# Performance work log

Hardware: AMD Instinct MI355X
Metric: run time of the kernel (lower is better)

The kernel has to match this reference:

```python
import jax, jax.numpy as jnp
from jax import lax
import numpy as np

B, DIM, H, W = 32, 256, 64, 64
HEADS = 4


def _dwconv(x, w, b, pad):
    # depthwise conv: w is (gc, 1, kh, kw), feature_group_count = gc
    y = lax.conv_general_dilated(x, w, window_strides=(1, 1), padding=pad,
                                 feature_group_count=w.shape[0])
    return y + b[None, :, None, None]


def setup_inputs() -> dict:
    key = jax.random.key(0)
    ks = jax.random.split(key, 9)
    gc = (DIM // 2) // 8  # branch_ratio = 0.125 -> 16
    s = 0.1
    return {
        "x": jax.random.normal(ks[0], (B, DIM, H, W), dtype=jnp.float32),
        "w_hw": jax.random.normal(ks[1], (gc, 1, 3, 3), dtype=jnp.float32) * s,
        "b_hw": jax.random.normal(ks[2], (gc,), dtype=jnp.float32) * s,
        "w_w": jax.random.normal(ks[3], (gc, 1, 1, 11), dtype=jnp.float32) * s,
        "b_w": jax.random.normal(ks[4], (gc,), dtype=jnp.float32) * s,
        "w_h": jax.random.normal(ks[5], (gc, 1, 11, 1), dtype=jnp.float32) * s,
        "b_h": jax.random.normal(ks[6], (gc,), dtype=jnp.float32) * s,
        "w_qkvl": jax.random.normal(ks[7], (DIM // 4 * HEADS, DIM // 2), dtype=jnp.float32) * s,
        "b_qkvl": jax.random.normal(ks[8], (DIM // 4 * HEADS,), dtype=jnp.float32) * s,
    }


def reference(x, w_hw, b_hw, w_w, b_w, w_h, b_h, w_qkvl, b_qkvl):
    Bx, C, Hx, Wx = x.shape
    C4 = C // 4
    gc = w_hw.shape[0]
    n_id = C // 2 - 3 * gc
    x1, x2 = jnp.split(x, 2, axis=1)  # each (B, C/2, H, W)

    # --- local branch: Inception depthwise conv + GELU ---
    xid = x1[:, :n_id]
    xhw = x1[:, n_id:n_id + gc]
    xw = x1[:, n_id + gc:n_id + 2 * gc]
    xh = x1[:, n_id + 2 * gc:]
    x1 = jnp.concatenate([
        xid,
        _dwconv(xhw, w_hw, b_hw, ((1, 1), (1, 1))),
        _dwconv(xw, w_w, b_w, ((0, 0), (5, 5))),
        _dwconv(xh, w_h, b_h, ((5, 5), (0, 0))),
    ], axis=1)
    x1 = jax.nn.gelu(x1, approximate=False)

    # --- global branch: 1x1 conv -> GELU -> pooled channel attention ---
    x2 = jnp.einsum('bchw,oc->bohw', x2, w_qkvl) + b_qkvl[None, :, None, None]
    x2 = jax.nn.gelu(x2, approximate=False)
    x2 = x2.reshape(Bx, HEADS, C4, Hx, Wx)

    q = jnp.sum(x2[:, :HEADS - 3], axis=1)          # (B, C4, H, W)
    k = x2[:, HEADS - 3]                             # (B, C4, H, W)
    v = x2[:, HEADS - 2].reshape(Bx, C4, Hx * Wx)    # (B, C4, HW)
    lfeat = x2[:, HEADS - 1]                         # (B, C4, H, W)

    # AvgPool2d(k=3, s=2, p=1) with count_include_pad=True (torch default)
    qp = lax.reduce_window(q, 0.0, lax.add, (1, 1, 3, 3), (1, 1, 2, 2),
                           ((0, 0), (0, 0), (1, 1), (1, 1))) / 9.0
    # MaxPool2d(k=2, s=2, p=0)
    kp = lax.reduce_window(k, -jnp.inf, lax.max, (1, 1, 2, 2), (1, 1, 2, 2), 'VALID')

    qf = qp.reshape(Bx, C4, -1)  # (B, C4, Np)
    kf = kp.reshape(Bx, C4, -1)  # (B, C4, Np)

    qk = jnp.einsum('bcn,bdn->bcd', qf, kf)          # (B, C4, C4)
    attn = jax.nn.softmax(qk, axis=1)                # softmax over dim=1, as in torch
    # torch: softmax(qk,1).transpose(1,2) @ v  ==  einsum over c
    out = jnp.einsum('bcd,bcm->bdm', attn, v).reshape(Bx, C4, Hx, Wx)

    return jnp.concatenate([x1, lfeat, out], axis=1)
```

## Files before the change

### kernel.cpp

```cpp
#include <hip/hip_runtime.h>
#include <hip/hip_bf16.h>

constexpr int kB   = 32;
constexpr int kC   = 256;
constexpr int kHW  = 4096;
constexpr int kC4  = 64;
constexpr int kGC  = 16;
constexpr int kNID = 80;

__device__ __forceinline__ float gelu_exact(float x) {
    return 0.5f * x * (1.0f + erff(x * 0.70710678118654752440f));
}

__device__ __forceinline__ float4 gelu4(float4 v) {
    return make_float4(gelu_exact(v.x), gelu_exact(v.y), gelu_exact(v.z), gelu_exact(v.w));
}

__global__ __launch_bounds__(256) void init_kernel(float4* __restrict__ qp, float4* __restrict__ qkb)
{
    int bid = blockIdx.x;
    if (bid < 2048) {
        size_t i = (size_t)bid * 256 + threadIdx.x;
        qp[i] = make_float4(0.f, 0.f, 0.f, 0.f);
    } else {
        size_t i = (size_t)(bid - 2048) * 256 + threadIdx.x;
        qkb[i] = make_float4(0.f, 0.f, 0.f, 0.f);
    }
}

__global__ __launch_bounds__(256) void part1_kernel(
    const float* __restrict__ x,
    const float* __restrict__ w_hw, const float* __restrict__ b_hw,
    const float* __restrict__ w_w,  const float* __restrict__ b_w,
    const float* __restrict__ w_h,  const float* __restrict__ b_h,
    float* __restrict__ out)
{
    int bc = blockIdx.x;
    int b  = bc >> 7;
    int c  = bc & 127;
    const float4* xp4 = (const float4*)(x   + (size_t)(b * kC + c) * kHW);
    float4*       op4 = (float4*)      (out + (size_t)(b * kC + c) * kHW);
    int tid = threadIdx.x;

    if (c < kNID) {
        for (int q = tid; q < 1024; q += 256)
            op4[q] = gelu4(xp4[q]);
    } else if (c < kNID + kGC) {
        int g = c - kNID;
        float wv[9];
        #pragma unroll
        for (int j = 0; j < 9; ++j) wv[j] = w_hw[g * 9 + j];
        float bias = b_hw[g];
        for (int q = tid; q < 1024; q += 256) {
            int h = q >> 4, wq = q & 15;
            float ax = bias, ay = bias, az = bias, aw = bias;
            #pragma unroll
            for (int dy = -1; dy <= 1; ++dy) {
                int rr = h + dy;
                if ((unsigned)rr >= 64u) continue;
                int base = rr * 16;
                float  l  = (wq > 0)  ? xp4[base + wq - 1].w : 0.f;
                float4 Bv = xp4[base + wq];
                float  r  = (wq < 15) ? xp4[base + wq + 1].x : 0.f;
                float w0 = wv[(dy + 1) * 3 + 0];
                float w1 = wv[(dy + 1) * 3 + 1];
                float w2 = wv[(dy + 1) * 3 + 2];
                ax += w0 * l    + w1 * Bv.x + w2 * Bv.y;
                ay += w0 * Bv.x + w1 * Bv.y + w2 * Bv.z;
                az += w0 * Bv.y + w1 * Bv.z + w2 * Bv.w;
                aw += w0 * Bv.z + w1 * Bv.w + w2 * r;
            }
            op4[q] = make_float4(gelu_exact(ax), gelu_exact(ay), gelu_exact(az), gelu_exact(aw));
        }
    } else if (c < kNID + 2 * kGC) {
        int g = c - (kNID + kGC);
        float wv[11];
        #pragma unroll
        for (int j = 0; j < 11; ++j) wv[j] = w_w[g * 11 + j];
        float bias = b_w[g];
        for (int q = tid; q < 1024; q += 256) {
            int h = q >> 4, wq = q & 15;
            int base = h * 16;
            float f[20];
            #pragma unroll
            for (int m = 0; m < 5; ++m) {
                int qq = wq + m - 2;
                float4 v;
                if ((unsigned)qq < 16u) v = xp4[base + qq];
                else                    v = make_float4(0.f, 0.f, 0.f, 0.f);
                f[4 * m + 0] = v.x; f[4 * m + 1] = v.y;
                f[4 * m + 2] = v.z; f[4 * m + 3] = v.w;
            }
            float a0 = bias, a1 = bias, a2 = bias, a3 = bias;
            #pragma unroll
            for (int m = 0; m < 11; ++m) {
                float w = wv[m];
                a0 += w * f[m + 3];
                a1 += w * f[m + 4];
                a2 += w * f[m + 5];
                a3 += w * f[m + 6];
            }
            op4[q] = make_float4(gelu_exact(a0), gelu_exact(a1), gelu_exact(a2), gelu_exact(a3));
        }
    } else {
        int g = c - (kNID + 2 * kGC);
        float wv[11];
        #pragma unroll
        for (int j = 0; j < 11; ++j) wv[j] = w_h[g * 11 + j];
        float bias = b_h[g];
        for (int q = tid; q < 1024; q += 256) {
            int h = q >> 4, wq = q & 15;
            float a0 = bias, a1 = bias, a2 = bias, a3 = bias;
            #pragma unroll
            for (int m = 0; m < 11; ++m) {
                int rr = h + m - 5;
                if ((unsigned)rr < 64u) {
                    float4 v = xp4[rr * 16 + wq];
                    float w = wv[m];
                    a0 += w * v.x; a1 += w * v.y; a2 += w * v.z; a3 += w * v.w;
                }
            }
            op4[q] = make_float4(gelu_exact(a0), gelu_exact(a1), gelu_exact(a2), gelu_exact(a3));
        }
    }
}

__global__ __launch_bounds__(256, 3) void conv1x1_kernel(
    const float* __restrict__ x,
    const float* __restrict__ w_qkvl, const float* __restrict__ b_qkvl,
    float* __restrict__ qp, float* __restrict__ kp,
    float* __restrict__ out)
{
    __shared__ float Ws[32][64];
    __shared__ float Xs[32 * 256];
    int pb   = blockIdx.x;
    int p0   = pb * 256;
    int head = blockIdx.y;
    int o0   = head * 64;
    int b    = blockIdx.z;
    int t    = threadIdx.x;
    int og   = t >> 5;
    int tp   = t & 31;

    float acc[8][8] = {};
    for (int kc = 0; kc < 4; ++kc) {
        #pragma unroll
        for (int r = 0; r < 2; ++r) {
            int g = t + r * 256;
            int o = g & 63, kq = g >> 6;
            float4 w4 = *(const float4*)&w_qkvl[(size_t)(o0 + o) * 128 + kc * 32 + kq * 4];
            Ws[kq * 4 + 0][o] = w4.x;
            Ws[kq * 4 + 1][o] = w4.y;
            Ws[kq * 4 + 2][o] = w4.z;
            Ws[kq * 4 + 3][o] = w4.w;
        }
        #pragma unroll
        for (int r = 0; r < 8; ++r) {
            int g = t + r * 256;
            int k = g >> 6, cch = g & 63;
            int cph = (cch >> 1) + (cch & 1) * 32;
            *(float4*)&Xs[k * 256 + cph * 4] =
                *(const float4*)&x[(size_t)(b * kC + 128 + kc * 32 + k) * kHW + p0 + cch * 4];
        }
        __syncthreads();
        #pragma unroll 2
        for (int k = 0; k < 32; ++k) {
            const float* xrow = &Xs[k * 256];
            float4 wa = *(const float4*)&Ws[k][og * 8];
            float4 wb = *(const float4*)&Ws[k][og * 8 + 4];
            float4 xa = *(const float4*)&xrow[tp * 4];
            float4 xb = *(const float4*)&xrow[128 + tp * 4];
            float w8[8] = {wa.x, wa.y, wa.z, wa.w, wb.x, wb.y, wb.z, wb.w};
            float x8[8] = {xa.x, xa.y, xa.z, xa.w, xb.x, xb.y, xb.z, xb.w};
            #pragma unroll
            for (int i = 0; i < 8; ++i)
                #pragma unroll
                for (int j = 0; j < 8; ++j)
                    acc[i][j] += w8[i] * x8[j];
        }
        __syncthreads();
    }

    if (head < 2) {
        float* Ps = &Xs[0];
        int r  = tp >> 3;
        int m0 = (tp & 7) * 4;
        #pragma unroll
        for (int i = 0; i < 8; ++i) {
            int o = og * 8 + i;
            float bias = b_qkvl[o0 + o];
            float y[8];
            #pragma unroll
            for (int j = 0; j < 8; ++j) y[j] = gelu_exact(acc[i][j] + bias);
            float s[4];
            if (head == 0) {
                float left = __shfl_up(y[7], 1);
                if ((tp & 7) == 0) left = 0.0f;
                s[0] = left + y[0] + y[1];
                s[1] = y[1] + y[2] + y[3];
                s[2] = y[3] + y[4] + y[5];
                s[3] = y[5] + y[6] + y[7];
            } else {
                s[0] = fmaxf(y[0], y[1]);
                s[1] = fmaxf(y[2], y[3]);
                s[2] = fmaxf(y[4], y[5]);
                s[3] = fmaxf(y[6], y[7]);
            }
            *(float4*)&Ps[o * 128 + r * 32 + m0] = *(float4*)s;
        }
        __syncthreads();
        if (head == 0) {
            bool last = (pb == 15);
            for (int e = t; e < 2048; e += 256) {
                int o = e >> 5, m = e & 31;
                const float* P = &Ps[o * 128 + m];
                float pv0 = P[0], pv1 = P[32], pv2 = P[64], pv3 = P[96];
                float* dst = &qp[(((size_t)(b * kC4 + o)) << 10) + (2 * pb) * 32 + m];
                dst[32] = (pv1 + pv2 + pv3) * (1.0f / 9.0f);
                atomicAdd(dst, (pv0 + pv1) * (1.0f / 9.0f));
                if (!last) atomicAdd(dst + 64, pv3 * (1.0f / 9.0f));
            }
        } else {
            for (int e = t; e < 2048; e += 256) {
                int o = e >> 5, m = e & 31;
                const float* P = &Ps[o * 128 + m];
                float* dst = &kp[(((size_t)(b * kC4 + o)) << 10) + (2 * pb) * 32 + m];
                dst[0]  = fmaxf(P[0],  P[32]);
                dst[32] = fmaxf(P[64], P[96]);
            }
        }
    } else {
        int cbase = (head == 2) ? 192 : 128;
        #pragma unroll
        for (int i = 0; i < 8; ++i) {
            int o = og * 8 + i;
            float bias = b_qkvl[o0 + o];
            float4 ya = make_float4(gelu_exact(acc[i][0] + bias), gelu_exact(acc[i][1] + bias),
                                    gelu_exact(acc[i][2] + bias), gelu_exact(acc[i][3] + bias));
            float4 yb = make_float4(gelu_exact(acc[i][4] + bias), gelu_exact(acc[i][5] + bias),
                                    gelu_exact(acc[i][6] + bias), gelu_exact(acc[i][7] + bias));
            float* dst = &out[(size_t)(b * kC + cbase + o) * kHW + p0 + tp * 8];
            *(float4*)dst       = ya;
            *(float4*)(dst + 4) = yb;
        }
    }
}

__global__ __launch_bounds__(256) void qk_partial_kernel(
    const float* __restrict__ qp, const float* __restrict__ kp,
    float* __restrict__ qkb)
{
    __shared__ float qsT[128][65];
    __shared__ float ksT[128][65];
    int nb = blockIdx.x;
    int b  = blockIdx.y;
    int t  = threadIdx.x;
    int tc = t & 15;
    int td = t >> 4;

    #pragma unroll
    for (int r = 0; r < 8; ++r) {
        int g = t + r * 256;
        int ch = g >> 5, n4 = g & 31;
        float4 q4 = *(const float4*)&qp[(size_t)(b * 64 + ch) * 1024 + nb * 128 + n4 * 4];
        qsT[n4 * 4 + 0][ch] = q4.x;
        qsT[n4 * 4 + 1][ch] = q4.y;
        qsT[n4 * 4 + 2][ch] = q4.z;
        qsT[n4 * 4 + 3][ch] = q4.w;
        float4 k4 = *(const float4*)&kp[(size_t)(b * 64 + ch) * 1024 + nb * 128 + n4 * 4];
        ksT[n4 * 4 + 0][ch] = k4.x;
        ksT[n4 * 4 + 1][ch] = k4.y;
        ksT[n4 * 4 + 2][ch] = k4.z;
        ksT[n4 * 4 + 3][ch] = k4.w;
    }
    __syncthreads();

    float acc[4][4] = {};
    #pragma unroll 4
    for (int n = 0; n < 128; ++n) {
        float4 q4 = *(const float4*)&qsT[n][tc * 4];
        float4 k4 = *(const float4*)&ksT[n][td * 4];
        float qa[4] = {q4.x, q4.y, q4.z, q4.w};
        float ka[4] = {k4.x, k4.y, k4.z, k4.w};
        #pragma unroll
        for (int i = 0; i < 4; ++i)
            #pragma unroll
            for (int j = 0; j < 4; ++j)
                acc[i][j] += qa[i] * ka[j];
    }
    #pragma unroll
    for (int i = 0; i < 4; ++i)
        #pragma unroll
        for (int j = 0; j < 4; ++j)
            atomicAdd(&qkb[((size_t)b * 64 + tc * 4 + i) * 64 + td * 4 + j], acc[i][j]);
}

__global__ __launch_bounds__(256) void softmax_kernel(
    const float* __restrict__ qkb, float* __restrict__ attn)
{
    __shared__ float qk_s[64][65];
    __shared__ float mxs[64], sms[64];
    int b = blockIdx.x;
    int t = threadIdx.x;
    #pragma unroll
    for (int r = 0; r < 16; ++r) {
        int g = t + r * 256;
        qk_s[g >> 6][g & 63] = qkb[(size_t)b * 4096 + g];
    }
    __syncthreads();
    if (t < 64) {
        float m = -1e30f;
        #pragma unroll 4
        for (int cc = 0; cc < 64; ++cc) m = fmaxf(m, qk_s[cc][t]);
        float s = 0.f;
        #pragma unroll 4
        for (int cc = 0; cc < 64; ++cc) s += expf(qk_s[cc][t] - m);
        mxs[t] = m;
        sms[t] = 1.0f / s;
    }
    __syncthreads();
    #pragma unroll
    for (int r = 0; r < 16; ++r) {
        int g = t + r * 256;
        int c = g >> 6, d = g & 63;
        attn[(size_t)b * 4096 + g] = expf(qk_s[c][d] - mxs[d]) * sms[d];
    }
}

__global__ __launch_bounds__(256) void out2_kernel(
    const float* __restrict__ attn, float* __restrict__ out)
{
    __shared__ float at[64][64];
    int b = blockIdx.y;
    int t = threadIdx.x;
    #pragma unroll
    for (int r = 0; r < 4; ++r) {
        int g = t + r * 256;
        *(float4*)&at[g >> 4][(g & 15) * 4] = *(const float4*)&attn[(size_t)b * 4096 + g * 4];
    }
    __syncthreads();
    int m = blockIdx.x * 256 + t;
    float* vcol = out + (size_t)(b * kC + 192) * kHW + m;
    float acc[64] = {};
    for (int c8 = 0; c8 < 8; ++c8) {
        float v[8];
        #pragma unroll
        for (int j = 0; j < 8; ++j) v[j] = vcol[(size_t)(c8 * 8 + j) * kHW];
        #pragma unroll
        for (int j = 0; j < 8; ++j) {
            float vv = v[j];
            const float* arow = &at[c8 * 8 + j][0];
            #pragma unroll
            for (int d4 = 0; d4 < 16; ++d4) {
                float4 a = *(const float4*)&arow[d4 * 4];
                acc[d4 * 4 + 0] += a.x * vv;
                acc[d4 * 4 + 1] += a.y * vv;
                acc[d4 * 4 + 2] += a.z * vv;
                acc[d4 * 4 + 3] += a.w * vv;
            }
        }
    }
    #pragma unroll
    for (int d = 0; d < 64; ++d)
        vcol[(size_t)d * kHW] = acc[d];
}

extern "C" void kernel_launch(void* const* d_in, const int* in_sizes, int n_in,
                              void* d_out, int out_size, void* d_ws, size_t ws_size,
                              hipStream_t stream)
{
    const float* x      = (const float*)d_in[0];
    const float* w_hw   = (const float*)d_in[1];
    const float* b_hw   = (const float*)d_in[2];
    const float* w_w    = (const float*)d_in[3];
    const float* b_w    = (const float*)d_in[4];
    const float* w_h    = (const float*)d_in[5];
    const float* b_h    = (const float*)d_in[6];
    const float* w_qkvl = (const float*)d_in[7];
    const float* b_qkvl = (const float*)d_in[8];
    float* out = (float*)d_out;

    char* w = (char*)d_ws;
    float* qp   = (float*)w;  w += (size_t)kB * kC4 * 1024 * 4;
    float* kp   = (float*)w;  w += (size_t)kB * kC4 * 1024 * 4;
    float* attn = (float*)w;  w += (size_t)kB * kC4 * kC4 * 4;
    float* qkb  = (float*)w;  w += (size_t)kB * kC4 * kC4 * 4;

    init_kernel<<<dim3(2176), 256, 0, stream>>>((float4*)qp, (float4*)qkb);
    part1_kernel<<<dim3(kB * 128), 256, 0, stream>>>(x, w_hw, b_hw, w_w, b_w, w_h, b_h, out);
    conv1x1_kernel<<<dim3(16, 4, kB), 256, 0, stream>>>(x, w_qkvl, b_qkvl, qp, kp, out);
    qk_partial_kernel<<<dim3(8, kB), 256, 0, stream>>>(qp, kp, qkb);
    softmax_kernel<<<dim3(kB), 256, 0, stream>>>(qkb, attn);
    out2_kernel<<<dim3(16, kB), 256, 0, stream>>>(attn, out);
}
```

Measured before the change: 451.8 us.

## Pre-transpose 1x1 weights and read them wave-uniformly; drop LDS staging in out2

A small new kernel transposes the qkvl weight matrix into workspace, reusing the attn buffer before it is written. The 1x1 conv kernel then gives each wavefront 16 output channels and reads the weights straight from global memory with wave-uniform addresses (readfirstlane), so the weights can come through scalar or broadcast loads instead of an LDS tile. Each thread now covers 4 pixels × 16 channels, the Xs layout is no longer permuted, and the occupancy hint of 3 blocks is dropped. out2 loads attn straight from global memory instead of staging it in LDS, relying on uniform broadcast. The risks are heavier global or scalar load traffic in the inner loops and different register pressure.

```diff
diff --git a/kernel.cpp b/kernel.cpp
--- a/kernel.cpp
+++ b/kernel.cpp
@@ -26,6 +26,16 @@
         size_t i = (size_t)(bid - 2048) * 256 + threadIdx.x;
         qkb[i] = make_float4(0.f, 0.f, 0.f, 0.f);
     }
+}
+
+__global__ __launch_bounds__(256) void wt_kernel(
+    const float* __restrict__ w_qkvl, float* __restrict__ wT)
+{
+    int k0 = blockIdx.x * 8;
+    int o  = threadIdx.x;
+    #pragma unroll
+    for (int r = 0; r < 8; ++r)
+        wT[(size_t)(k0 + r) * 256 + o] = w_qkvl[(size_t)o * 128 + k0 + r];
 }
 
 __global__ __launch_bounds__(256) void part1_kernel(
@@ -125,88 +135,76 @@
     }
 }
 
-__global__ __launch_bounds__(256, 3) void conv1x1_kernel(
+__global__ __launch_bounds__(256) void conv1x1_kernel(
     const float* __restrict__ x,
-    const float* __restrict__ w_qkvl, const float* __restrict__ b_qkvl,
+    const float* __restrict__ wT, const float* __restrict__ b_qkvl,
     float* __restrict__ qp, float* __restrict__ kp,
     float* __restrict__ out)
 {
-    __shared__ float Ws[32][64];
     __shared__ float Xs[32 * 256];
     int pb   = blockIdx.x;
     int p0   = pb * 256;
     int head = blockIdx.y;
-    int o0   = head * 64;
     int b    = blockIdx.z;
     int t    = threadIdx.x;
-    int og   = t >> 5;
-    int tp   = t & 31;
-
-    float acc[8][8] = {};
+    int lane = t & 63;
+    int wvid = __builtin_amdgcn_readfirstlane(t >> 6);
+    int ow   = head * 64 + wvid * 16;
+
+    float acc[16][4] = {};
     for (int kc = 0; kc < 4; ++kc) {
-        #pragma unroll
-        for (int r = 0; r < 2; ++r) {
-            int g = t + r * 256;
-            int o = g & 63, kq = g >> 6;
-            float4 w4 = *(const float4*)&w_qkvl[(size_t)(o0 + o) * 128 + kc * 32 + kq * 4];
-            Ws[kq * 4 + 0][o] = w4.x;
-            Ws[kq * 4 + 1][o] = w4.y;
-            Ws[kq * 4 + 2][o] = w4.z;
-            Ws[kq * 4 + 3][o] = w4.w;
-        }
         #pragma unroll
         for (int r = 0; r < 8; ++r) {
             int g = t + r * 256;
             int k = g >> 6, cch = g & 63;
-            int cph = (cch >> 1) + (cch & 1) * 32;
-            *(float4*)&Xs[k * 256 + cph * 4] =
+            *(float4*)&Xs[k * 256 + cch * 4] =
                 *(const float4*)&x[(size_t)(b * kC + 128 + kc * 32 + k) * kHW + p0 + cch * 4];
         }
         __syncthreads();
-        #pragma unroll 2
+        #pragma unroll 4
         for (int k = 0; k < 32; ++k) {
-            const float* xrow = &Xs[k * 256];
-            float4 wa = *(const float4*)&Ws[k][og * 8];
-            float4 wb = *(const float4*)&Ws[k][og * 8 + 4];
-            float4 xa = *(const float4*)&xrow[tp * 4];
-            float4 xb = *(const float4*)&xrow[128 + tp * 4];
-            float w8[8] = {wa.x, wa.y, wa.z, wa.w, wb.x, wb.y, wb.z, wb.w};
-            float x8[8] = {xa.x, xa.y, xa.z, xa.w, xb.x, xb.y, xb.z, xb.w};
-            #pragma unroll
-            for (int i = 0; i < 8; ++i)
+            const float* wr = wT + (size_t)(kc * 32 + k) * 256 + ow;
+            float4 w0 = *(const float4*)&wr[0];
+            float4 w1 = *(const float4*)&wr[4];
+            float4 w2 = *(const float4*)&wr[8];
+            float4 w3 = *(const float4*)&wr[12];
+            float4 xv = *(const float4*)&Xs[k * 256 + lane * 4];
+            float wv[16] = {w0.x, w0.y, w0.z, w0.w, w1.x, w1.y, w1.z, w1.w,
+                            w2.x, w2.y, w2.z, w2.w, w3.x, w3.y, w3.z, w3.w};
+            float xa[4] = {xv.x, xv.y, xv.z, xv.w};
+            #pragma unroll
+            for (int i = 0; i < 16; ++i)
                 #pragma unroll
-                for (int j = 0; j < 8; ++j)
-                    acc[i][j] += w8[i] * x8[j];
+                for (int j = 0; j < 4; ++j)
+                    acc[i][j] += wv[i] * xa[j];
         }
         __syncthreads();
     }
 
     if (head < 2) {
         float* Ps = &Xs[0];
-        int r  = tp >> 3;
-        int m0 = (tp & 7) * 4;
-        #pragma unroll
-        for (int i = 0; i < 8; ++i) {
-            int o = og * 8 + i;
-            float bias = b_qkvl[o0 + o];
-            float y[8];
-            #pragma unroll
-            for (int j = 0; j < 8; ++j) y[j] = gelu_exact(acc[i][j] + bias);
-            float s[4];
+        int r  = lane >> 4;
+        int m0 = 2 * (lane & 15);
+        #pragma unroll
+        for (int i = 0; i < 16; ++i) {
+            int o = wvid * 16 + i;
+            float bias = b_qkvl[ow + i];
+            float y0 = gelu_exact(acc[i][0] + bias);
+            float y1 = gelu_exact(acc[i][1] + bias);
+            float y2 = gelu_exact(acc[i][2] + bias);
+            float y3 = gelu_exact(acc[i][3] + bias);
+            float s0, s1;
             if (head == 0) {
-                float left = __shfl_up(y[7], 1);
-                if ((tp & 7) == 0) left = 0.0f;
-                s[0] = left + y[0] + y[1];
-                s[1] = y[1] + y[2] + y[3];
-                s[2] = y[3] + y[4] + y[5];
-                s[3] = y[5] + y[6] + y[7];
+                float left = __shfl_up(y3, 1);
+                if ((lane & 15) == 0) left = 0.0f;
+                s0 = left + y0 + y1;
+                s1 = y1 + y2 + y3;
             } else {
-                s[0] = fmaxf(y[0], y[1]);
-                s[1] = fmaxf(y[2], y[3]);
-                s[2] = fmaxf(y[4], y[5]);
-                s[3] = fmaxf(y[6], y[7]);
-            }
-            *(float4*)&Ps[o * 128 + r * 32 + m0] = *(float4*)s;
+                s0 = fmaxf(y0, y1);
+                s1 = fmaxf(y2, y3);
+            }
+            Ps[o * 128 + r * 32 + m0]     = s0;
+            Ps[o * 128 + r * 32 + m0 + 1] = s1;
         }
         __syncthreads();
         if (head == 0) {
@@ -230,18 +228,14 @@
             }
         }
     } else {
-        int cbase = (head == 2) ? 192 : 128;
-        #pragma unroll
-        for (int i = 0; i < 8; ++i) {
-            int o = og * 8 + i;
-            float bias = b_qkvl[o0 + o];
-            float4 ya = make_float4(gelu_exact(acc[i][0] + bias), gelu_exact(acc[i][1] + bias),
-                                    gelu_exact(acc[i][2] + bias), gelu_exact(acc[i][3] + bias));
-            float4 yb = make_float4(gelu_exact(acc[i][4] + bias), gelu_exact(acc[i][5] + bias),
-                                    gelu_exact(acc[i][6] + bias), gelu_exact(acc[i][7] + bias));
-            float* dst = &out[(size_t)(b * kC + cbase + o) * kHW + p0 + tp * 8];
-            *(float4*)dst       = ya;
-            *(float4*)(dst + 4) = yb;
+        #pragma unroll
+        for (int i = 0; i < 16; ++i) {
+            int og  = ow + i;
+            int och = (head == 2) ? (og + 64) : (og - 64);
+            float bias = b_qkvl[og];
+            float4 y = make_float4(gelu_exact(acc[i][0] + bias), gelu_exact(acc[i][1] + bias),
+                                   gelu_exact(acc[i][2] + bias), gelu_exact(acc[i][3] + bias));
+            *(float4*)&out[(size_t)(b * kC + och) * kHW + p0 + lane * 4] = y;
         }
     }
 }
@@ -330,35 +324,19 @@
 __global__ __launch_bounds__(256) void out2_kernel(
     const float* __restrict__ attn, float* __restrict__ out)
 {
-    __shared__ float at[64][64];
     int b = blockIdx.y;
     int t = threadIdx.x;
-    #pragma unroll
-    for (int r = 0; r < 4; ++r) {
-        int g = t + r * 256;
-        *(float4*)&at[g >> 4][(g & 15) * 4] = *(const float4*)&attn[(size_t)b * 4096 + g * 4];
-    }
-    __syncthreads();
     int m = blockIdx.x * 256 + t;
     float* vcol = out + (size_t)(b * kC + 192) * kHW + m;
+    const float* ar = attn + (size_t)b * 4096;
     float acc[64] = {};
-    for (int c8 = 0; c8 < 8; ++c8) {
-        float v[8];
-        #pragma unroll
-        for (int j = 0; j < 8; ++j) v[j] = vcol[(size_t)(c8 * 8 + j) * kHW];
-        #pragma unroll
-        for (int j = 0; j < 8; ++j) {
-            float vv = v[j];
-            const float* arow = &at[c8 * 8 + j][0];
-            #pragma unroll
-            for (int d4 = 0; d4 < 16; ++d4) {
-                float4 a = *(const float4*)&arow[d4 * 4];
-                acc[d4 * 4 + 0] += a.x * vv;
-                acc[d4 * 4 + 1] += a.y * vv;
-                acc[d4 * 4 + 2] += a.z * vv;
-                acc[d4 * 4 + 3] += a.w * vv;
-            }
-        }
+    #pragma unroll 2
+    for (int c = 0; c < 64; ++c) {
+        float vv = vcol[(size_t)c * kHW];
+        const float* arow = ar + c * 64;
+        #pragma unroll
+        for (int d = 0; d < 64; ++d)
+            acc[d] += arow[d] * vv;
     }
     #pragma unroll
     for (int d = 0; d < 64; ++d)
@@ -385,10 +363,12 @@
     float* kp   = (float*)w;  w += (size_t)kB * kC4 * 1024 * 4;
     float* attn = (float*)w;  w += (size_t)kB * kC4 * kC4 * 4;
     float* qkb  = (float*)w;  w += (size_t)kB * kC4 * kC4 * 4;
+    float* wT   = attn;
 
     init_kernel<<<dim3(2176), 256, 0, stream>>>((float4*)qp, (float4*)qkb);
+    wt_kernel<<<dim3(16), 256, 0, stream>>>(w_qkvl, wT);
     part1_kernel<<<dim3(kB * 128), 256, 0, stream>>>(x, w_hw, b_hw, w_w, b_w, w_h, b_h, out);
-    conv1x1_kernel<<<dim3(16, 4, kB), 256, 0, stream>>>(x, w_qkvl, b_qkvl, qp, kp, out);
+    conv1x1_kernel<<<dim3(16, 4, kB), 256, 0, stream>>>(x, wT, b_qkvl, qp, kp, out);
     qk_partial_kernel<<<dim3(8, kB), 256, 0, stream>>>(qp, kp, qkb);
     softmax_kernel<<<dim3(kB), 256, 0, stream>>>(qkb, attn);
     out2_kernel<<<dim3(16, kB), 256, 0, stream>>>(attn, out);
```

Result: faster. 426.6 us (-5.6%).
